# Kernel optimization log

Hardware: AMD Instinct MI355X
Metric: run time of the kernel (lower is better)

Reference implementation:

```python
import jax, jax.numpy as jnp
import numpy as np

B, N, F, K, NK, MID = 64, 100, 2048, 16, 8, 1024


def setup_inputs() -> dict:
    key = jax.random.key(0)
    ks = jax.random.split(key, 10)
    v = jax.random.normal(ks[0], (B, N, F), dtype=jnp.float32)
    v_mask = jnp.ones((B, N), dtype=jnp.float32)
    coord = jax.random.normal(ks[1], (B, N, N, 2), dtype=jnp.float32)
    adj_matrix = jax.random.uniform(ks[2], (B, N, K), dtype=jnp.float32)
    top_ind = jax.random.randint(ks[3], (B, N, K), 0, N)
    mean_rho = jax.random.uniform(ks[4], (NK,), minval=0.0, maxval=1.0)
    mean_theta = jax.random.uniform(ks[5], (NK,), minval=-np.pi, maxval=np.pi)
    precision_rho = jax.random.uniform(ks[6], (NK,), minval=0.0, maxval=1.0)
    precision_theta = jax.random.uniform(ks[7], (NK,), minval=0.0, maxval=1.0)
    # stacked per-kernel Linear weights: [NK, MID//NK, F] (no bias)
    W = jax.random.normal(ks[8], (NK, MID // NK, F), dtype=jnp.float32) * 0.02
    return {"v": v, "v_mask": v_mask, "coord": coord, "adj_matrix": adj_matrix,
            "top_ind": top_ind, "mean_rho": mean_rho, "mean_theta": mean_theta,
            "precision_rho": precision_rho, "precision_theta": precision_theta, "W": W}


def _gaussian_weights(coord, mean_rho, mean_theta, precision_rho, precision_theta):
    # coord: [B, N, N, 2] -> weights [B, N, N, NK], normalized over kernel axis
    rho = coord[..., 0][..., None]    # [B,N,N,1]
    theta = coord[..., 1][..., None]  # [B,N,N,1]
    w_rho = jnp.exp(-0.5 * (rho - mean_rho) ** 2 / (1e-14 + precision_rho ** 2))
    first_angle = jnp.abs(theta - mean_theta)
    second_angle = jnp.abs(2.0 * np.pi - first_angle)
    w_theta = jnp.exp(-0.5 * jnp.minimum(first_angle, second_angle) ** 2
                      / (1e-14 + precision_theta ** 2))
    w = w_rho * w_theta
    w = jnp.where(jnp.isnan(w), 0.0, w)
    # torch code normalizes the (-1, NK) view over dim=1 == kernel axis
    return w / (jnp.sum(w, axis=-1, keepdims=True) + 1e-14)


def reference(v, v_mask, coord, adj_matrix, top_ind,
              mean_rho, mean_theta, precision_rho, precision_theta, W):
    coord_weight = _gaussian_weights(coord, mean_rho, mean_theta,
                                     precision_rho, precision_theta)  # [B,N,N,NK]
    # gather top-K neighbor features: sparse_v[b,i,k] = v[b, top_ind[b,i,k]]
    sparse_v = jax.vmap(lambda vb, idx: vb[idx])(v, top_ind)           # [B,N,K,F]
    # gather corresponding Gaussian weights along neighbor axis
    sparse_weight = jnp.take_along_axis(coord_weight, top_ind[..., None], axis=2)  # [B,N,K,NK]
    attentive_v = sparse_v * adj_matrix[..., None]                     # weight_adj=True
    # weighted_neighbourhood = sparse_weight^T @ attentive_v : [B,N,NK,F]
    wn = jnp.einsum('bnkm,bnkf->bnmf', sparse_weight, attentive_v)
    # per-kernel linear then concat over kernels -> [B,N,NK*(MID//NK)]
    out = jnp.einsum('bnmf,mof->bnmo', wn, W)
    return out.reshape(v.shape[0], v.shape[1], -1)
```

## Files before the change

### kernel.cpp

```cpp
#include <hip/hip_runtime.h>
#include <math.h>

#define Bc 64
#define Nc 100
#define Fc 2048
#define Kc 16
#define NKc 8
#define BN (Bc*Nc)
#define MO 1024
#define TWO_PI 6.283185307179586f

typedef __attribute__((ext_vector_type(8))) short bf16x8;
typedef __attribute__((ext_vector_type(4))) float f32x4;

__device__ __forceinline__ unsigned short f2bf(float x) {
    union { float f; unsigned u; } c; c.f = x;
    unsigned r = c.u + 0x7FFFu + ((c.u >> 16) & 1u);
    return (unsigned short)(r >> 16);
}
__device__ __forceinline__ float bf2f(unsigned short x) {
    return __uint_as_float((unsigned)x << 16);
}

__global__ __launch_bounds__(256) void prep(
    const float* __restrict__ v, const float* __restrict__ W,
    unsigned short* __restrict__ dst, int n8v, int nCvt,
    const float* __restrict__ coord, const float* __restrict__ adj,
    const int* __restrict__ top_ind,
    const float* __restrict__ mean_rho, const float* __restrict__ mean_theta,
    const float* __restrict__ prec_rho, const float* __restrict__ prec_theta,
    float* __restrict__ aw)
{
    const int bid = blockIdx.x;
    const int tid = threadIdx.x;
    if (bid < nCvt) {
        const int i = bid * 256 + tid;
        const float* src = (i < n8v) ? (v + (size_t)i * 8)
                                     : (W + (size_t)(i - n8v) * 8);
        const float4 x0 = ((const float4*)src)[0];
        const float4 x1 = ((const float4*)src)[1];
        bf16x8 o;
        o[0]=(short)f2bf(x0.x); o[1]=(short)f2bf(x0.y);
        o[2]=(short)f2bf(x0.z); o[3]=(short)f2bf(x0.w);
        o[4]=(short)f2bf(x1.x); o[5]=(short)f2bf(x1.y);
        o[6]=(short)f2bf(x1.z); o[7]=(short)f2bf(x1.w);
        *(bf16x8*)(dst + (size_t)i * 8) = o;
        return;
    }
    __shared__ int   idx[2][Kc];
    __shared__ float wv[2][Kc][NKc];
    __shared__ float sc[2][Kc];
    const int h  = tid >> 7;
    const int t7 = tid & 127;
    const int bn = (bid - nCvt) * 2 + h;
    if (t7 < Kc) idx[h][t7] = top_ind[bn * Kc + t7];
    __syncthreads();
    const int k = t7 >> 3, m = t7 & 7;
    const int j = idx[h][k];
    const float rho   = coord[((size_t)bn * Nc + j) * 2 + 0];
    const float theta = coord[((size_t)bn * Nc + j) * 2 + 1];
    const float dr = rho - mean_rho[m];
    const float pr = prec_rho[m];
    const float wr = expf(-0.5f * dr * dr / (1e-14f + pr * pr));
    const float fa = fabsf(theta - mean_theta[m]);
    const float sa = fabsf(TWO_PI - fa);
    const float da = fminf(fa, sa);
    const float pt = prec_theta[m];
    const float wt = expf(-0.5f * da * da / (1e-14f + pt * pt));
    float w = wr * wt;
    if (w != w) w = 0.0f;
    wv[h][k][m] = w;
    __syncthreads();
    if (t7 < Kc) {
        float s = 0.f;
        #pragma unroll
        for (int mm = 0; mm < NKc; ++mm) s += wv[h][t7][mm];
        sc[h][t7] = adj[bn * Kc + t7] / (s + 1e-14f);
    }
    __syncthreads();
    aw[(size_t)bn * 128 + m * 16 + k] = wv[h][k][m] * sc[h][k];
}

#define GBM 112
#define GBN 128
#define GBK 64
#define NT (Fc/GBK)
#define A_OFF   0
#define A_BUF   14336
#define B_OFF   28672
#define B_BUF   16384
#define IDX_OFF 30720
#define AW_OFF  37120

#define SYNC() do { asm volatile("s_waitcnt vmcnt(0)" ::: "memory"); \
                    __builtin_amdgcn_s_barrier(); \
                    __builtin_amdgcn_sched_barrier(0); } while (0)

template<int MI>
__device__ __forceinline__ void compute_tile(
    f32x4 (&acc)[4][2], const unsigned char* smem,
    int buf, int wm, int wn, int fr, int kg, int rsw)
{
    #pragma unroll
    for (int kk = 0; kk < 2; ++kk) {
        bf16x8 af[MI], bfr[2];
        #pragma unroll
        for (int mi = 0; mi < MI; ++mi)
            af[mi] = *(const bf16x8*)(smem + A_OFF + buf * A_BUF
                        + (wm * 64 + mi * 16 + fr) * 128
                        + ((kk * 32 + kg) ^ rsw) * 2);
        #pragma unroll
        for (int ni = 0; ni < 2; ++ni)
            bfr[ni] = *(const bf16x8*)(smem + B_OFF + buf * B_BUF
                        + (wn * 32 + ni * 16 + fr) * 128
                        + ((kk * 32 + kg) ^ rsw) * 2);
        #pragma unroll
        for (int mi = 0; mi < MI; ++mi)
            #pragma unroll
            for (int ni = 0; ni < 2; ++ni)
                acc[mi][ni] = __builtin_amdgcn_mfma_f32_16x16x32_bf16(
                    af[mi], bfr[ni], acc[mi][ni], 0, 0, 0);
    }
}

__global__ __launch_bounds__(512, 4) void gemm_fused(
    const unsigned short* __restrict__ A,
    const unsigned short* __restrict__ B,
    const float* __restrict__ aw,
    const int* __restrict__ top_ind,
    float* __restrict__ out)
{
    __shared__ __align__(16) unsigned char smem[61440];

    const int tid = threadIdx.x;
    const int w  = tid >> 6, l = tid & 63;
    const int wm = w >> 2;
    const int wn = w & 3;
    const int bid = blockIdx.x;
    const int xcd  = bid & 7;
    const int slot = bid >> 3;
    const int b  = xcd * 8 + (slot >> 3);
    const int jt = slot & 7;
    const int i0 = b * Nc;
    const int j0 = jt * GBN;

    const int srow = tid >> 3;
    const int scol = 8 * ((l & 7) ^ (l >> 3));

    const int fr = l & 15;
    const int kg = (l >> 4) * 8;
    const int rsw = 8 * (fr & 7);

    f32x4 acc[4][2] = {};

    auto stage = [&](int buf, int t) {
        const size_t k0 = (size_t)t * GBK;
        #pragma unroll
        for (int q = 0; q < 2; ++q) {
            const int row = q * 64 + srow;
            __builtin_amdgcn_global_load_lds(
                (const __attribute__((address_space(1))) void*)
                    (B + (size_t)(j0 + row) * Fc + k0 + scol),
                (__attribute__((address_space(3))) void*)
                    (smem + B_OFF + buf * B_BUF + q * 8192 + w * 1024),
                16, 0, 0);
        }
        {
            const int row = i0 + srow;
            __builtin_amdgcn_global_load_lds(
                (const __attribute__((address_space(1))) void*)
                    (A + (size_t)row * Fc + k0 + scol),
                (__attribute__((address_space(3))) void*)
                    (smem + A_OFF + buf * A_BUF + w * 1024),
                16, 0, 0);
        }
        {
            int row = i0 + 48 + srow;
            if (row > BN - 1) row = BN - 1;
            __builtin_amdgcn_global_load_lds(
                (const __attribute__((address_space(1))) void*)
                    (A + (size_t)row * Fc + k0 + scol),
                (__attribute__((address_space(3))) void*)
                    (smem + A_OFF + buf * A_BUF + 6144 + w * 1024),
                16, 0, 0);
        }
    };

    #define COMPUTE(buf) do { \
        if (wm == 0) compute_tile<4>(acc, smem, (buf), wm, wn, fr, kg, rsw); \
        else         compute_tile<3>(acc, smem, (buf), wm, wn, fr, kg, rsw); \
    } while (0)

    stage(0, 0);
    SYNC();
    int t = 0;
    for (; t + 2 < NT; t += 2) {
        stage(1, t + 1);  COMPUTE(0);  SYNC();
        stage(0, t + 2);  COMPUTE(1);  SYNC();
    }
    stage(1, NT - 1);  COMPUTE(0);  SYNC();
    COMPUTE(1);

    __syncthreads();
    const int cn = l & 15;
    const int cr = (l >> 4) * 4;
    const int MIw = 4 - wm;
    #pragma unroll
    for (int mi = 0; mi < 4; ++mi) {
        if (mi < MIw) {
            #pragma unroll
            for (int ni = 0; ni < 2; ++ni) {
                #pragma unroll
                for (int r = 0; r < 4; ++r) {
                    const int row = wm * 64 + mi * 16 + cr + r;
                    const int col = wn * 32 + ni * 16 + cn;
                    *(unsigned short*)(smem + row * 264 + col * 2) =
                        f2bf(acc[mi][ni][r]);
                }
            }
        }
    }
    for (int i = tid; i < Nc * Kc; i += 512) {
        ((int*)(smem + IDX_OFF))[i] = top_ind[(size_t)b * Nc * Kc + i];
        ((float*)(smem + AW_OFF))[i] =
            aw[(size_t)(b * Nc + (i >> 4)) * 128 + jt * 16 + (i & 15)];
    }
    __syncthreads();

    const int cq = tid & 31;
    for (int n = tid >> 5; n < Nc; n += 16) {
        float4 o = make_float4(0.f, 0.f, 0.f, 0.f);
        #pragma unroll
        for (int k = 0; k < Kc; ++k) {
            const int   r = ((const int*)(smem + IDX_OFF))[n * Kc + k];
            const float a = ((const float*)(smem + AW_OFF))[n * Kc + k];
            const ushort4 u = *(const ushort4*)(smem + r * 264 + cq * 8);
            o.x += a * bf2f(u.x); o.y += a * bf2f(u.y);
            o.z += a * bf2f(u.z); o.w += a * bf2f(u.w);
        }
        *(float4*)&out[(size_t)(b * Nc + n) * MO + j0 + cq * 4] = o;
    }
}

#define TM 64
#define TN 64
#define FBK 16

__device__ __forceinline__ void compute_a(
    int bn, int tid,
    const float* __restrict__ coord, const float* __restrict__ adj,
    const int* __restrict__ top_ind,
    const float* __restrict__ mean_rho, const float* __restrict__ mean_theta,
    const float* __restrict__ prec_rho, const float* __restrict__ prec_theta,
    int (&lds_idx)[Kc], float (&lds_a)[Kc][NKc], float (&lds_scale)[Kc])
{
    if (tid < Kc) lds_idx[tid] = top_ind[bn * Kc + tid];
    __syncthreads();
    if (tid < Kc * NKc) {
        const int k = tid >> 3, m = tid & 7;
        const int j = lds_idx[k];
        const float rho   = coord[((size_t)bn * Nc + j) * 2 + 0];
        const float theta = coord[((size_t)bn * Nc + j) * 2 + 1];
        const float dr = rho - mean_rho[m];
        const float pr = prec_rho[m];
        const float wr = expf(-0.5f * dr * dr / (1e-14f + pr * pr));
        const float fa = fabsf(theta - mean_theta[m]);
        const float sa = fabsf(TWO_PI - fa);
        const float da = fminf(fa, sa);
        const float pt = prec_theta[m];
        const float wt = expf(-0.5f * da * da / (1e-14f + pt * pt));
        float w = wr * wt;
        if (w != w) w = 0.0f;
        lds_a[k][m] = w;
    }
    __syncthreads();
    if (tid < Kc) {
        float s = 0.f;
        #pragma unroll
        for (int m = 0; m < NKc; ++m) s += lds_a[tid][m];
        lds_scale[tid] = adj[bn * Kc + tid] / (s + 1e-14f);
    }
    __syncthreads();
    if (tid < Kc * NKc) {
        const int k = tid >> 3, m = tid & 7;
        lds_a[k][m] *= lds_scale[k];
    }
    __syncthreads();
}

__global__ __launch_bounds__(256) void gemm_p(
    const float* __restrict__ A,
    const float* __restrict__ Bm,
    float* __restrict__ P)
{
    __shared__ float At[FBK][TM + 4];
    __shared__ float Bt[FBK][TN + 4];
    const int tid = threadIdx.x;
    const int tx = tid & 15;
    const int ty = tid >> 4;
    const int i0 = blockIdx.x * TM;
    const int j0 = blockIdx.y * TN;
    const int lk = tid & 15;
    const int lr = tid >> 4;

    float acc[4][4] = {};

    for (int k0 = 0; k0 < Fc; k0 += FBK) {
        #pragma unroll
        for (int rr = 0; rr < 4; ++rr) {
            At[lk][lr + rr * 16] = A[(size_t)(i0 + lr + rr * 16) * Fc + k0 + lk];
            Bt[lk][lr + rr * 16] = Bm[(size_t)(j0 + lr + rr * 16) * Fc + k0 + lk];
        }
        __syncthreads();
        #pragma unroll
        for (int kk = 0; kk < FBK; ++kk) {
            float a4[4], b4[4];
            #pragma unroll
            for (int p = 0; p < 4; ++p) a4[p] = At[kk][ty * 4 + p];
            #pragma unroll
            for (int p = 0; p < 4; ++p) b4[p] = Bt[kk][tx * 4 + p];
            #pragma unroll
            for (int pi = 0; pi < 4; ++pi)
                #pragma unroll
                for (int pj = 0; pj < 4; ++pj)
                    acc[pi][pj] += a4[pi] * b4[pj];
        }
        __syncthreads();
    }

    #pragma unroll
    for (int pi = 0; pi < 4; ++pi)
        #pragma unroll
        for (int pj = 0; pj < 4; ++pj)
            P[(size_t)(i0 + ty * 4 + pi) * MO + j0 + tx * 4 + pj] = acc[pi][pj];
}

__global__ __launch_bounds__(256) void combine_f32(
    const float* __restrict__ P,
    const float* __restrict__ coord, const float* __restrict__ adj,
    const int* __restrict__ top_ind,
    const float* __restrict__ mr, const float* __restrict__ mt,
    const float* __restrict__ pr, const float* __restrict__ pt,
    float* __restrict__ out)
{
    __shared__ int   lds_idx[Kc];
    __shared__ float lds_a[Kc][NKc];
    __shared__ float lds_scale[Kc];
    const int bn = blockIdx.x;
    const int tid = threadIdx.x;
    const int b = bn / Nc;

    compute_a(bn, tid, coord, adj, top_ind, mr, mt, pr, pt,
              lds_idx, lds_a, lds_scale);

    const int m = tid >> 5;
    float ak[Kc];
    size_t rowoff[Kc];
    #pragma unroll
    for (int k = 0; k < Kc; ++k) {
        ak[k] = lds_a[k][m];
        rowoff[k] = (size_t)(b * Nc + lds_idx[k]) * MO + tid * 4;
    }
    float4 acc = make_float4(0.f, 0.f, 0.f, 0.f);
    #pragma unroll
    for (int k = 0; k < Kc; ++k) {
        const float4 p = *(const float4*)&P[rowoff[k]];
        acc.x += ak[k] * p.x; acc.y += ak[k] * p.y;
        acc.z += ak[k] * p.z; acc.w += ak[k] * p.w;
    }
    *(float4*)&out[(size_t)bn * MO + tid * 4] = acc;
}

extern "C" void kernel_launch(void* const* d_in, const int* in_sizes, int n_in,
                              void* d_out, int out_size, void* d_ws, size_t ws_size,
                              hipStream_t stream) {
    const float* v        = (const float*)d_in[0];
    const float* coord    = (const float*)d_in[2];
    const float* adj      = (const float*)d_in[3];
    const int*   top_ind  = (const int*)d_in[4];
    const float* mr       = (const float*)d_in[5];
    const float* mt       = (const float*)d_in[6];
    const float* pr       = (const float*)d_in[7];
    const float* pt       = (const float*)d_in[8];
    const float* W        = (const float*)d_in[9];
    float* out = (float*)d_out;

    const size_t vbBytes = (size_t)BN * Fc * sizeof(unsigned short);
    const size_t WbBytes = (size_t)MO * Fc * sizeof(unsigned short);
    const size_t awBytes = (size_t)BN * 128 * sizeof(float);
    const size_t needBF  = vbBytes + WbBytes + awBytes;
    const size_t PBytes  = (size_t)BN * MO * sizeof(float);

    if (ws_size >= needBF) {
        char* ws = (char*)d_ws;
        unsigned short* vb = (unsigned short*)ws;
        unsigned short* Wb = vb + (size_t)BN * Fc;
        float* aw          = (float*)(ws + vbBytes + WbBytes);

        const int n8v   = BN * Fc / 8;
        const int nCvt  = (n8v + MO * Fc / 8) / 256;
        const int nWgt  = BN / 2;
        prep<<<nCvt + nWgt, 256, 0, stream>>>(v, W, vb, n8v, nCvt,
                                              coord, adj, top_ind,
                                              mr, mt, pr, pt, aw);

        gemm_fused<<<512, 512, 0, stream>>>(vb, Wb, aw, top_ind, out);
    } else if (ws_size >= PBytes) {
        float* P = (float*)d_ws;
        gemm_p<<<dim3(BN / TM, MO / TN), 256, 0, stream>>>(v, W, P);
        combine_f32<<<BN, 256, 0, stream>>>(P, coord, adj, top_ind,
                                            mr, mt, pr, pt, out);
    }
}
```

Baseline: 58.78 us.

## Fuse fp32-to-bf16 conversion of v into GEMM A-tile loading

The separate pre-pass that converted the whole activation tensor v to bf16 in workspace is removed. The GEMM now loads fp32 A rows directly into registers, converts them to bf16 and writes them into swizzled LDS, prefetching one tile ahead while B still uses direct global-to-LDS loads. This drops a full write and reread of the bf16 copy of v, but doubles the bytes read for A in the GEMM (fp32 instead of bf16). Because A is re-read by the 8 column-tile blocks, it also adds register-staged conversion work and LDS store latency to the main loop.

```diff
diff --git a/kernel.cpp b/kernel.cpp
--- a/kernel.cpp
+++ b/kernel.cpp
@@ -23,8 +23,7 @@
 }
 
 __global__ __launch_bounds__(256) void prep(
-    const float* __restrict__ v, const float* __restrict__ W,
-    unsigned short* __restrict__ dst, int n8v, int nCvt,
+    const float* __restrict__ W, unsigned short* __restrict__ Wb, int nCvt,
     const float* __restrict__ coord, const float* __restrict__ adj,
     const int* __restrict__ top_ind,
     const float* __restrict__ mean_rho, const float* __restrict__ mean_theta,
@@ -35,16 +34,14 @@
     const int tid = threadIdx.x;
     if (bid < nCvt) {
         const int i = bid * 256 + tid;
-        const float* src = (i < n8v) ? (v + (size_t)i * 8)
-                                     : (W + (size_t)(i - n8v) * 8);
-        const float4 x0 = ((const float4*)src)[0];
-        const float4 x1 = ((const float4*)src)[1];
+        const float4 x0 = ((const float4*)(W + (size_t)i * 8))[0];
+        const float4 x1 = ((const float4*)(W + (size_t)i * 8))[1];
         bf16x8 o;
         o[0]=(short)f2bf(x0.x); o[1]=(short)f2bf(x0.y);
         o[2]=(short)f2bf(x0.z); o[3]=(short)f2bf(x0.w);
         o[4]=(short)f2bf(x1.x); o[5]=(short)f2bf(x1.y);
         o[6]=(short)f2bf(x1.z); o[7]=(short)f2bf(x1.w);
-        *(bf16x8*)(dst + (size_t)i * 8) = o;
+        *(bf16x8*)(Wb + (size_t)i * 8) = o;
         return;
     }
     __shared__ int   idx[2][Kc];
@@ -92,10 +89,6 @@
 #define IDX_OFF 30720
 #define AW_OFF  37120
 
-#define SYNC() do { asm volatile("s_waitcnt vmcnt(0)" ::: "memory"); \
-                    __builtin_amdgcn_s_barrier(); \
-                    __builtin_amdgcn_sched_barrier(0); } while (0)
-
 template<int MI>
 __device__ __forceinline__ void compute_tile(
     f32x4 (&acc)[4][2], const unsigned char* smem,
@@ -124,7 +117,7 @@
 }
 
 __global__ __launch_bounds__(512, 4) void gemm_fused(
-    const unsigned short* __restrict__ A,
+    const float* __restrict__ Af,
     const unsigned short* __restrict__ B,
     const float* __restrict__ aw,
     const int* __restrict__ top_ind,
@@ -145,15 +138,31 @@
     const int j0 = jt * GBN;
 
     const int srow = tid >> 3;
+    const int cg   = tid & 7;
     const int scol = 8 * ((l & 7) ^ (l >> 3));
 
     const int fr = l & 15;
     const int kg = (l >> 4) * 8;
     const int rsw = 8 * (fr & 7);
 
+    const int aswz = (((cg) ^ (srow & 7)) << 4);
+    unsigned char* const adst = smem + A_OFF + srow * 128 + aswz;
+
     f32x4 acc[4][2] = {};
 
-    auto stage = [&](int buf, int t) {
+    auto loadA = [&](int t, float4& ra0, float4& ra1, float4& rb0, float4& rb1) {
+        const size_t k0 = (size_t)t * GBK;
+        const float* pa = Af + (size_t)(i0 + srow) * Fc + k0 + cg * 8;
+        ra0 = *(const float4*)pa;
+        ra1 = *(const float4*)(pa + 4);
+        int r2 = i0 + 48 + srow;
+        if (r2 > BN - 1) r2 = BN - 1;
+        const float* pb = Af + (size_t)r2 * Fc + k0 + cg * 8;
+        rb0 = *(const float4*)pb;
+        rb1 = *(const float4*)(pb + 4);
+    };
+
+    auto stageB = [&](int buf, int t) {
         const size_t k0 = (size_t)t * GBK;
         #pragma unroll
         for (int q = 0; q < 2; ++q) {
@@ -165,25 +174,20 @@
                     (smem + B_OFF + buf * B_BUF + q * 8192 + w * 1024),
                 16, 0, 0);
         }
-        {
-            const int row = i0 + srow;
-            __builtin_amdgcn_global_load_lds(
-                (const __attribute__((address_space(1))) void*)
-                    (A + (size_t)row * Fc + k0 + scol),
-                (__attribute__((address_space(3))) void*)
-                    (smem + A_OFF + buf * A_BUF + w * 1024),
-                16, 0, 0);
-        }
-        {
-            int row = i0 + 48 + srow;
-            if (row > BN - 1) row = BN - 1;
-            __builtin_amdgcn_global_load_lds(
-                (const __attribute__((address_space(1))) void*)
-                    (A + (size_t)row * Fc + k0 + scol),
-                (__attribute__((address_space(3))) void*)
-                    (smem + A_OFF + buf * A_BUF + 6144 + w * 1024),
-                16, 0, 0);
-        }
+    };
+
+    auto writeA = [&](int buf, float4 ra0, float4 ra1, float4 rb0, float4 rb1) {
+        bf16x8 w1, w2;
+        w1[0]=(short)f2bf(ra0.x); w1[1]=(short)f2bf(ra0.y);
+        w1[2]=(short)f2bf(ra0.z); w1[3]=(short)f2bf(ra0.w);
+        w1[4]=(short)f2bf(ra1.x); w1[5]=(short)f2bf(ra1.y);
+        w1[6]=(short)f2bf(ra1.z); w1[7]=(short)f2bf(ra1.w);
+        w2[0]=(short)f2bf(rb0.x); w2[1]=(short)f2bf(rb0.y);
+        w2[2]=(short)f2bf(rb0.z); w2[3]=(short)f2bf(rb0.w);
+        w2[4]=(short)f2bf(rb1.x); w2[5]=(short)f2bf(rb1.y);
+        w2[6]=(short)f2bf(rb1.z); w2[7]=(short)f2bf(rb1.w);
+        *(bf16x8*)(adst + buf * A_BUF)        = w1;
+        *(bf16x8*)(adst + buf * A_BUF + 6144) = w2;
     };
 
     #define COMPUTE(buf) do { \
@@ -191,17 +195,35 @@
         else         compute_tile<3>(acc, smem, (buf), wm, wn, fr, kg, rsw); \
     } while (0)
 
-    stage(0, 0);
-    SYNC();
-    int t = 0;
-    for (; t + 2 < NT; t += 2) {
-        stage(1, t + 1);  COMPUTE(0);  SYNC();
-        stage(0, t + 2);  COMPUTE(1);  SYNC();
-    }
-    stage(1, NT - 1);  COMPUTE(0);  SYNC();
-    COMPUTE(1);
-
-    __syncthreads();
+    {
+        float4 ra0, ra1, rb0, rb1;
+        loadA(0, ra0, ra1, rb0, rb1);
+        stageB(0, 0);
+        asm volatile("s_waitcnt vmcnt(0)" ::: "memory");
+        writeA(0, ra0, ra1, rb0, rb1);
+        __syncthreads();
+    }
+
+    int buf = 0;
+    #pragma unroll 2
+    for (int t = 0; t < NT; ++t) {
+        float4 na0, na1, nb0, nb1;
+        const bool more = (t + 1 < NT);
+        if (more) {
+            loadA(t + 1, na0, na1, nb0, nb1);
+            stageB(buf ^ 1, t + 1);
+        }
+        __builtin_amdgcn_sched_barrier(0);
+        COMPUTE(buf);
+        __builtin_amdgcn_sched_barrier(0);
+        if (more) {
+            asm volatile("s_waitcnt vmcnt(0)" ::: "memory");
+            writeA(buf ^ 1, na0, na1, nb0, nb1);
+        }
+        __syncthreads();
+        buf ^= 1;
+    }
+
     const int cn = l & 15;
     const int cr = (l >> 4) * 4;
     const int MIw = 4 - wm;
@@ -385,26 +407,23 @@
     const float* W        = (const float*)d_in[9];
     float* out = (float*)d_out;
 
-    const size_t vbBytes = (size_t)BN * Fc * sizeof(unsigned short);
     const size_t WbBytes = (size_t)MO * Fc * sizeof(unsigned short);
     const size_t awBytes = (size_t)BN * 128 * sizeof(float);
-    const size_t needBF  = vbBytes + WbBytes + awBytes;
+    const size_t needBF  = WbBytes + awBytes;
     const size_t PBytes  = (size_t)BN * MO * sizeof(float);
 
     if (ws_size >= needBF) {
         char* ws = (char*)d_ws;
-        unsigned short* vb = (unsigned short*)ws;
-        unsigned short* Wb = vb + (size_t)BN * Fc;
-        float* aw          = (float*)(ws + vbBytes + WbBytes);
-
-        const int n8v   = BN * Fc / 8;
-        const int nCvt  = (n8v + MO * Fc / 8) / 256;
-        const int nWgt  = BN / 2;
-        prep<<<nCvt + nWgt, 256, 0, stream>>>(v, W, vb, n8v, nCvt,
+        unsigned short* Wb = (unsigned short*)ws;
+        float* aw          = (float*)(ws + WbBytes);
+
+        const int nCvt = (MO * Fc / 8) / 256;
+        const int nWgt = BN / 2;
+        prep<<<nCvt + nWgt, 256, 0, stream>>>(W, Wb, nCvt,
                                               coord, adj, top_ind,
                                               mr, mt, pr, pt, aw);
 
-        gemm_fused<<<512, 512, 0, stream>>>(vb, Wb, aw, top_ind, out);
+        gemm_fused<<<512, 512, 0, stream>>>(v, Wb, aw, top_ind, out);
     } else if (ws_size >= PBytes) {
         float* P = (float*)d_ws;
         gemm_p<<<dim3(BN / TM, MO / TN), 256, 0, stream>>>(v, W, P);
```

Result: slower. 61.05 us, median of 2 (+3.9%).

## Split K across waves with 64x64 per-wave tiles and LDS partial reduction

Applied to the files above, without the earlier changes.

The eight waves are regrouped from a 2x4 M/N grid into a 2x2x2 grid, with a split along K. Each wave now computes a 64x64 output tile over half of every 64-wide K step, so it issues fewer LDS fragment loads per MFMA. The two K-halves write bf16 partial tiles into separate LDS regions, and the gather epilogue sums them. The epilogue also reads top_ind and aw straight from global memory instead of staging them in LDS. The costs are more accumulator registers per wave, an extra LDS read per gathered row, and rounding of each partial to bf16 before the sum.

```diff
diff --git a/kernel.cpp b/kernel.cpp
--- a/kernel.cpp
+++ b/kernel.cpp
@@ -89,8 +89,8 @@
 #define A_BUF   14336
 #define B_OFF   28672
 #define B_BUF   16384
-#define IDX_OFF 30720
-#define AW_OFF  37120
+#define P0_OFF  0
+#define P1_OFF  30720
 
 #define SYNC() do { asm volatile("s_waitcnt vmcnt(0)" ::: "memory"); \
                     __builtin_amdgcn_s_barrier(); \
@@ -98,29 +98,26 @@
 
 template<int MI>
 __device__ __forceinline__ void compute_tile(
-    f32x4 (&acc)[4][2], const unsigned char* smem,
-    int buf, int wm, int wn, int fr, int kg, int rsw)
-{
-    #pragma unroll
-    for (int kk = 0; kk < 2; ++kk) {
-        bf16x8 af[MI], bfr[2];
-        #pragma unroll
-        for (int mi = 0; mi < MI; ++mi)
-            af[mi] = *(const bf16x8*)(smem + A_OFF + buf * A_BUF
-                        + (wm * 64 + mi * 16 + fr) * 128
-                        + ((kk * 32 + kg) ^ rsw) * 2);
-        #pragma unroll
-        for (int ni = 0; ni < 2; ++ni)
-            bfr[ni] = *(const bf16x8*)(smem + B_OFF + buf * B_BUF
-                        + (wn * 32 + ni * 16 + fr) * 128
-                        + ((kk * 32 + kg) ^ rsw) * 2);
-        #pragma unroll
-        for (int mi = 0; mi < MI; ++mi)
-            #pragma unroll
-            for (int ni = 0; ni < 2; ++ni)
-                acc[mi][ni] = __builtin_amdgcn_mfma_f32_16x16x32_bf16(
-                    af[mi], bfr[ni], acc[mi][ni], 0, 0, 0);
-    }
+    f32x4 (&acc)[4][4], const unsigned char* smem,
+    int buf, int wm, int wn, int kcol)
+{
+    const int fr_row = 0;
+    (void)fr_row;
+    bf16x8 af[MI], bfr[4];
+    #pragma unroll
+    for (int mi = 0; mi < MI; ++mi)
+        af[mi] = *(const bf16x8*)(smem + A_OFF + buf * A_BUF
+                    + (wm * 64 + mi * 16) * 128 + kcol + (kcol >> 31));
+    #pragma unroll
+    for (int ni = 0; ni < 4; ++ni)
+        bfr[ni] = *(const bf16x8*)(smem + B_OFF + buf * B_BUF
+                    + (wn * 64 + ni * 16) * 128 + kcol);
+    #pragma unroll
+    for (int mi = 0; mi < MI; ++mi)
+        #pragma unroll
+        for (int ni = 0; ni < 4; ++ni)
+            acc[mi][ni] = __builtin_amdgcn_mfma_f32_16x16x32_bf16(
+                af[mi], bfr[ni], acc[mi][ni], 0, 0, 0);
 }
 
 __global__ __launch_bounds__(512, 4) void gemm_fused(
@@ -134,8 +131,9 @@
 
     const int tid = threadIdx.x;
     const int w  = tid >> 6, l = tid & 63;
-    const int wm = w >> 2;
-    const int wn = w & 3;
+    const int wm = (w >> 2) & 1;
+    const int wn = (w >> 1) & 1;
+    const int wk = w & 1;
     const int bid = blockIdx.x;
     const int xcd  = bid & 7;
     const int slot = bid >> 3;
@@ -150,8 +148,9 @@
     const int fr = l & 15;
     const int kg = (l >> 4) * 8;
     const int rsw = 8 * (fr & 7);
-
-    f32x4 acc[4][2] = {};
+    const int kcol = (((wk * 32 + kg) ^ rsw) * 2) + fr * 128;
+
+    f32x4 acc[4][4] = {};
 
     auto stage = [&](int buf, int t) {
         const size_t k0 = (size_t)t * GBK;
@@ -187,8 +186,8 @@
     };
 
     #define COMPUTE(buf) do { \
-        if (wm == 0) compute_tile<4>(acc, smem, (buf), wm, wn, fr, kg, rsw); \
-        else         compute_tile<3>(acc, smem, (buf), wm, wn, fr, kg, rsw); \
+        if (wm == 0) compute_tile<4>(acc, smem, (buf), wm, wn, kcol); \
+        else         compute_tile<3>(acc, smem, (buf), wm, wn, kcol); \
     } while (0)
 
     stage(0, 0);
@@ -205,38 +204,39 @@
     const int cn = l & 15;
     const int cr = (l >> 4) * 4;
     const int MIw = 4 - wm;
+    unsigned char* const pbase = smem + (wk ? P1_OFF : P0_OFF);
     #pragma unroll
     for (int mi = 0; mi < 4; ++mi) {
         if (mi < MIw) {
             #pragma unroll
-            for (int ni = 0; ni < 2; ++ni) {
+            for (int ni = 0; ni < 4; ++ni) {
                 #pragma unroll
                 for (int r = 0; r < 4; ++r) {
                     const int row = wm * 64 + mi * 16 + cr + r;
-                    const int col = wn * 32 + ni * 16 + cn;
-                    *(unsigned short*)(smem + row * 264 + col * 2) =
+                    const int col = wn * 64 + ni * 16 + cn;
+                    *(unsigned short*)(pbase + row * 264 + col * 2) =
                         f2bf(acc[mi][ni][r]);
                 }
             }
         }
     }
-    for (int i = tid; i < Nc * Kc; i += 512) {
-        ((int*)(smem + IDX_OFF))[i] = top_ind[(size_t)b * Nc * Kc + i];
-        ((float*)(smem + AW_OFF))[i] =
-            aw[(size_t)(b * Nc + (i >> 4)) * 128 + jt * 16 + (i & 15)];
-    }
     __syncthreads();
 
     const int cq = tid & 31;
+    const int* tib = top_ind + (size_t)b * Nc * Kc;
+    const float* awb = aw + (size_t)b * Nc * 128 + jt * 16;
     for (int n = tid >> 5; n < Nc; n += 16) {
         float4 o = make_float4(0.f, 0.f, 0.f, 0.f);
         #pragma unroll
         for (int k = 0; k < Kc; ++k) {
-            const int   r = ((const int*)(smem + IDX_OFF))[n * Kc + k];
-            const float a = ((const float*)(smem + AW_OFF))[n * Kc + k];
-            const ushort4 u = *(const ushort4*)(smem + r * 264 + cq * 8);
-            o.x += a * bf2f(u.x); o.y += a * bf2f(u.y);
-            o.z += a * bf2f(u.z); o.w += a * bf2f(u.w);
+            const int   r = tib[n * Kc + k];
+            const float a = awb[(size_t)n * 128 + k];
+            const ushort4 u0 = *(const ushort4*)(smem + P0_OFF + r * 264 + cq * 8);
+            const ushort4 u1 = *(const ushort4*)(smem + P1_OFF + r * 264 + cq * 8);
+            o.x += a * (bf2f(u0.x) + bf2f(u1.x));
+            o.y += a * (bf2f(u0.y) + bf2f(u1.y));
+            o.z += a * (bf2f(u0.z) + bf2f(u1.z));
+            o.w += a * (bf2f(u0.w) + bf2f(u1.w));
         }
         *(float4*)&out[(size_t)(b * Nc + n) * MO + j0 + cq * 4] = o;
     }
```

New measurement: 166.1 us. 2.83x slower.
